# Kernel optimization log

Hardware: AMD Instinct MI355X
Metric: run time of the kernel (lower is better)

Reference implementation:

```python
import jax, jax.numpy as jnp
import numpy as np

B, C, H, W = 2, 64, 256, 256
DW = 128          # c * DW_Expand
FFN = 128         # c * FFN_Expand
GRID = 8          # wH = wW modulation grid


def setup_inputs() -> dict:
    key = jax.random.key(0)
    ks = jax.random.split(key, 16)
    rn = lambda k, s, sc=1.0: jax.random.normal(k, s, jnp.float32) * sc
    return {
        "x": rn(ks[0], (B, C, H, W)),
        "w1": rn(ks[1], (DW, C), (2.0 / C) ** 0.5),
        "b1": jnp.zeros((DW,), jnp.float32),
        "w2": rn(ks[2], (DW, 3, 3), (2.0 / 9.0) ** 0.5),
        "b2": jnp.zeros((DW,), jnp.float32),
        "w3": rn(ks[3], (C, DW // 2), (2.0 / (DW // 2)) ** 0.5),
        "b3": jnp.zeros((C,), jnp.float32),
        "sca_w": rn(ks[4], (DW // 2, DW // 2), (1.0 / (DW // 2)) ** 0.5),
        "sca_b": jnp.zeros((DW // 2,), jnp.float32),
        "w4": rn(ks[5], (FFN, C), (2.0 / C) ** 0.5),
        "b4": jnp.zeros((FFN,), jnp.float32),
        "w5": rn(ks[6], (C, FFN // 2), (2.0 / (FFN // 2)) ** 0.5),
        "b5": jnp.zeros((C,), jnp.float32),
        "n1_w": jnp.ones((C,), jnp.float32),
        "n1_b": jnp.zeros((C,), jnp.float32),
        "n2_w": jnp.ones((C,), jnp.float32),
        "n2_b": jnp.zeros((C,), jnp.float32),
        "beta": rn(ks[7], (C,), 0.1),
        "gamma": rn(ks[8], (C,), 0.1),
        "mod1": rn(ks[9], (B, DW, C, GRID, GRID)),
        "mod2": rn(ks[10], (B, DW, GRID, GRID)),
        "mod3": rn(ks[11], (B, C, DW // 2, GRID, GRID)),
        "mod4": rn(ks[12], (B, FFN, C, GRID, GRID)),
        "mod5": rn(ks[13], (B, C, FFN // 2, GRID, GRID)),
    }


def layernorm2d(x, w, b, eps=1e-6):
    # channel-wise LayerNorm per pixel (NAFNet LayerNorm2d)
    mu = jnp.mean(x, axis=1, keepdims=True)
    var = jnp.mean((x - mu) ** 2, axis=1, keepdims=True)
    return (x - mu) / jnp.sqrt(var + eps) * w[None, :, None, None] + b[None, :, None, None]


def conv1x1_modulated(x, wb, bb, mod):
    # wb: [Co,Ci], mod: [B,Co,Ci,wH,wW]; per-patch 1x1 conv with normalized dynamic weights
    w = wb[None, :, :, None, None] * mod                      # [B,Co,Ci,wH,wW]
    w = w / jnp.sqrt(jnp.sum(w * w, axis=2, keepdims=True))   # normalize over Ci (kh*kw==1)
    b_, ci, h, wd = x.shape
    wh, ww = mod.shape[-2:]
    ph, pw = h // wh, wd // ww
    xp = x.reshape(b_, ci, wh, ph, ww, pw)                    # split into patches
    y = jnp.einsum('bocuv,bcupvq->boupvq', w, xp)             # per-patch matmul
    return y.reshape(b_, wb.shape[0], h, wd) + bb[None, :, None, None]


def conv3x3_dw_modulated(x, wb, bb, mod):
    # wb: [C,3,3], mod: [B,C,wH,wW]; per-patch depthwise 3x3, padding 1 across whole image
    w = wb[None, :, :, :, None, None] * mod[:, :, None, None, :, :]  # [B,C,3,3,wH,wW]
    w = w / jnp.sqrt(jnp.sum(w * w, axis=(2, 3), keepdims=True))     # normalize over (ci=1, kh*kw)
    b_, c, h, wd = x.shape
    wh, ww = mod.shape[-2:]
    ph, pw = h // wh, wd // ww
    xpad = jnp.pad(x, ((0, 0), (0, 0), (1, 1), (1, 1)))
    out = jnp.zeros_like(x)
    for dh in range(3):
        for dw_ in range(3):
            xs = xpad[:, :, dh:dh + h, dw_:dw_ + wd].reshape(b_, c, wh, ph, ww, pw)
            wk = w[:, :, dh, dw_, :, :]                        # [B,C,wH,wW]
            out = out + (wk[:, :, :, None, :, None] * xs).reshape(b_, c, h, wd)
    return out + bb[None, :, None, None]


def simple_gate(x):
    a, g = jnp.split(x, 2, axis=1)
    return a * g


def reference(x, w1, b1, w2, b2, w3, b3, sca_w, sca_b, w4, b4, w5, b5,
              n1_w, n1_b, n2_w, n2_b, beta, gamma, mod1, mod2, mod3, mod4, mod5):
    y = layernorm2d(x, n1_w, n1_b)
    y = conv1x1_modulated(y, w1, b1, mod1)
    y = conv3x3_dw_modulated(y, w2, b2, mod2)
    y = simple_gate(y)
    s = jnp.mean(y, axis=(2, 3), keepdims=True)               # SCA: global pool + 1x1
    s = jnp.einsum('oc,bcij->boij', sca_w, s) + sca_b[None, :, None, None]
    y = y * s
    y = conv1x1_modulated(y, w3, b3, mod3)
    y1 = x + y * beta[None, :, None, None]
    z = conv1x1_modulated(layernorm2d(y1, n2_w, n2_b), w4, b4, mod4)
    z = simple_gate(z)
    z = conv1x1_modulated(z, w5, b5, mod5)
    return y1 + z * gamma[None, :, None, None]
```

## Files before the change

kernel.cpp:

```cpp
#include <hip/hip_runtime.h>
#include <hip/hip_bf16.h>


typedef __bf16 bf16x8 __attribute__((ext_vector_type(8)));
typedef float f32x4 __attribute__((ext_vector_type(4)));
typedef unsigned short u16x8 __attribute__((ext_vector_type(8)));

__device__ __forceinline__ float b2f(unsigned short u) {
    union { unsigned int i; float f; } x; x.i = ((unsigned int)u) << 16; return x.f;
}
__device__ __forceinline__ unsigned short f2b(float f) {
    union { float f; unsigned int i; } x; x.f = f;
    unsigned int i = x.i;
    return (unsigned short)((i + 0x7FFFu + ((i >> 16) & 1u)) >> 16);
}
__device__ __forceinline__ unsigned int pk2(float a, float b) {
    __hip_bfloat162 h = __float22bfloat162_rn(float2{a, b});
    union { __hip_bfloat162 h; unsigned int u; } cv; cv.h = h; return cv.u;
}

__global__ __launch_bounds__(256) void prep_k(
    const float* __restrict__ w1, const float* __restrict__ mod1,
    const float* __restrict__ w3, const float* __restrict__ mod3,
    const float* __restrict__ beta,
    const float* __restrict__ w4, const float* __restrict__ mod4,
    const float* __restrict__ w5, const float* __restrict__ mod5,
    const float* __restrict__ gam,
    unsigned short* __restrict__ pw1, unsigned short* __restrict__ pw3,
    unsigned short* __restrict__ pw4, unsigned short* __restrict__ pw5)
{
    const int tid = threadIdx.x;
    int blk = blockIdx.x;
    const float* w; const float* mod; const float* rows = nullptr;
    unsigned short* out; int NOUT; int rem;
    if (blk < 256)      { w = w1; mod = mod1; out = pw1; NOUT = 128; rem = blk; }
    else if (blk < 384) { w = w3; mod = mod3; out = pw3; NOUT = 64;  rem = blk - 256; rows = beta; }
    else if (blk < 640) { w = w4; mod = mod4; out = pw4; NOUT = 128; rem = blk - 384; }
    else                { w = w5; mod = mod5; out = pw5; NOUT = 64;  rem = blk - 640; rows = gam;
                          if (out == nullptr) return; }
    const int b = rem / NOUT, o = rem % NOUT;

    __shared__ float mlds[64 * 68];
    __shared__ float wlsh[64];
    __shared__ float red[4 * 64];
    __shared__ float rs[64];

    const float* mbase = mod + ((size_t)(b * NOUT + o) * 64) * 64;
#pragma unroll
    for (int k = 0; k < 4; ++k) {
        int l = tid + k * 256;
        float4 vv = ((const float4*)mbase)[l];
        int c = l >> 4, q = l & 15;
        *(float4*)&mlds[c * 68 + q * 4] = vv;
    }
    if (tid < 64) wlsh[tid] = w[o * 64 + tid];
    __syncthreads();

    {
        int uv = tid & 63, part = tid >> 6;
        float ss = 0.f;
#pragma unroll
        for (int j = 0; j < 16; ++j) {
            int c = part * 16 + j;
            float t = wlsh[c] * mlds[c * 68 + uv];
            ss += t * t;
        }
        red[part * 64 + uv] = ss;
    }
    __syncthreads();
    if (tid < 64) {
        float tot = red[tid] + red[64 + tid] + red[128 + tid] + red[192 + tid];
        float rv = rows ? rows[o] : 1.f;
        rs[tid] = rsqrtf(fmaxf(tot, 1e-30f)) * rv;
    }
    __syncthreads();

    {
        int uvw = tid >> 2, cp = tid & 3;
        float r = rs[uvw];
        size_t obase = ((size_t)(b * 64 + uvw) * NOUT + o) * 64;
#pragma unroll
        for (int g = 0; g < 2; ++g) {
            u16x8 pk;
#pragma unroll
            for (int e = 0; e < 8; ++e) {
                int c = cp * 16 + g * 8 + e;
                pk[e] = f2b(wlsh[c] * mlds[c * 68 + uvw] * r);
            }
            *(u16x8*)&out[obase + cp * 16 + g * 8] = pk;
        }
    }
}

template <int NOUT, bool LN, bool GATE, bool RESID, bool SCALE_IN,
          bool IN_F32, bool RES_F32, bool OUT_F32, bool PREPPED>
__global__ __launch_bounds__(256, 2) void conv_k(
    const void* __restrict__ in_,
    void* __restrict__ out_,
    const unsigned short* __restrict__ pw,
    const float* __restrict__ wb,
    const float* __restrict__ mod,
    const float* __restrict__ bias,
    const float* __restrict__ lnw,
    const float* __restrict__ lnb,
    const void* __restrict__ resid_,
    const float* __restrict__ rows,
    const float* __restrict__ svec,
    int bbase)
{
    constexpr int CHOUT = GATE ? 64 : NOUT;
    constexpr int PARTS = 256 / NOUT;
    constexpr int CP    = 64 / PARTS;

    const int tid   = threadIdx.x;
    const int chunk = blockIdx.x;
    const int uv    = blockIdx.y;
    const int z     = blockIdx.z;
    const int bfull = z + bbase;
    const int u = uv >> 3, v = uv & 7;
    const int h_base = u * 32 + chunk * 4;
    const int w_base = v * 32;

    __shared__ __align__(16) unsigned short stage[128 * 72];
    __shared__ __align__(16) unsigned short wlds[NOUT * 72];
    __shared__ float sbias[NOUT];
    __shared__ float shP[PREPPED ? 1 : 256];

    const int o_p  = tid & (NOUT - 1);
    const int part = tid / NOUT;
    float wv[PREPPED ? 1 : CP];
    if constexpr (PREPPED) {
        const unsigned short* pwb = pw + ((size_t)(bfull * 64 + uv) * NOUT) * 64;
#pragma unroll
        for (int k = 0; k < NOUT / 32; ++k) {
            int ci = tid + k * 256;
            *(u16x8*)&wlds[(ci >> 3) * 72 + (ci & 7) * 8] = *(const u16x8*)&pwb[ci * 8];
        }
        if (tid < NOUT) {
            float bs = bias[tid];
            if constexpr (RESID) bs *= rows[tid];
            sbias[tid] = bs;
        }
    } else {
        float ss = 0.f;
#pragma unroll
        for (int j = 0; j < CP; ++j) {
            int c = part * CP + j;
            wv[j] = wb[o_p * 64 + c] * mod[(((bfull * NOUT + o_p) * 64 + c) << 6) + uv];
            ss += wv[j] * wv[j];
        }
        shP[o_p * PARTS + part] = ss;
    }

    const int cg = tid & 7;
    const int qd = tid >> 3;
    const int c0 = cg * 8;
    const int pixg = (h_base + (qd >> 3)) * 256 + w_base + (qd & 7) * 4;
    float v2[8][4];
#pragma unroll
    for (int k = 0; k < 8; ++k) {
        int idx = ((z * 64 + c0 + k) << 16) + pixg;
        if constexpr (IN_F32) {
            float4 t = *(const float4*)&((const float*)in_)[idx];
            v2[k][0] = t.x; v2[k][1] = t.y; v2[k][2] = t.z; v2[k][3] = t.w;
        } else {
            ushort4 t = *(const ushort4*)&((const unsigned short*)in_)[idx];
            v2[k][0] = b2f(t.x); v2[k][1] = b2f(t.y); v2[k][2] = b2f(t.z); v2[k][3] = b2f(t.w);
        }
    }
    float mu[4], rstd[4];
    if constexpr (LN) {
#pragma unroll
        for (int e = 0; e < 4; ++e) {
            float s1 = 0.f, s2 = 0.f;
#pragma unroll
            for (int k = 0; k < 8; ++k) { s1 += v2[k][e]; s2 += v2[k][e] * v2[k][e]; }
#pragma unroll
            for (int m = 1; m < 8; m <<= 1) {
                s1 += __shfl_xor(s1, m);
                s2 += __shfl_xor(s2, m);
            }
            mu[e] = s1 * (1.f / 64.f);
            float var = s2 * (1.f / 64.f) - mu[e] * mu[e];
            rstd[e] = rsqrtf(fmaxf(var, 0.f) + 1e-6f);
        }
    }
    float lw[8], lb[8], sv[8];
    if constexpr (LN) {
        *(float4*)&lw[0] = *(const float4*)&lnw[c0];
        *(float4*)&lw[4] = *(const float4*)&lnw[c0 + 4];
        *(float4*)&lb[0] = *(const float4*)&lnb[c0];
        *(float4*)&lb[4] = *(const float4*)&lnb[c0 + 4];
    }
    if constexpr (SCALE_IN) {
        *(float4*)&sv[0] = *(const float4*)&svec[bfull * 64 + c0];
        *(float4*)&sv[4] = *(const float4*)&svec[bfull * 64 + c0 + 4];
    }
#pragma unroll
    for (int e = 0; e < 4; ++e) {
        float o8[8];
#pragma unroll
        for (int k = 0; k < 8; ++k) {
            float val = v2[k][e];
            if constexpr (LN) val = (val - mu[e]) * rstd[e] * lw[k] + lb[k];
            if constexpr (SCALE_IN) val *= sv[k];
            o8[k] = val;
        }
        uint4 pk;
        pk.x = pk2(o8[0], o8[1]); pk.y = pk2(o8[2], o8[3]);
        pk.z = pk2(o8[4], o8[5]); pk.w = pk2(o8[6], o8[7]);
        *(uint4*)&stage[(qd * 4 + e) * 72 + c0] = pk;
    }

    __syncthreads();

    if constexpr (!PREPPED) {
        float tot = 0.f;
#pragma unroll
        for (int k = 0; k < PARTS; ++k) tot += shP[o_p * PARTS + k];
        float rn = rsqrtf(fmaxf(tot, 1e-30f));
        float rsv = 1.f;
        if constexpr (RESID) { rsv = rows[o_p]; rn *= rsv; }
#pragma unroll
        for (int j = 0; j < CP; ++j)
            wlds[o_p * 72 + part * CP + j] = f2b(wv[j] * rn);
        if (part == 0) {
            float bs = bias[o_p];
            if constexpr (RESID) bs *= rsv;
            sbias[o_p] = bs;
        }
        __syncthreads();
    }

    const int wave = tid >> 6;
    const int lane = tid & 63;
    const int q = lane >> 4;
    const int r = lane & 15;

    constexpr int NF = (NOUT == 64) ? 1 : 2;
    int nfi[2];
    if constexpr (NOUT == 64)      { nfi[0] = wave;     nfi[1] = wave; }
    else if constexpr (GATE)       { nfi[0] = wave;     nfi[1] = wave + 4; }
    else                           { nfi[0] = 2 * wave; nfi[1] = 2 * wave + 1; }

    bf16x8 bfr[NF][2];
#pragma unroll
    for (int f = 0; f < NF; ++f)
#pragma unroll
        for (int ks = 0; ks < 2; ++ks)
            bfr[f][ks] = *(const bf16x8*)&wlds[(16 * nfi[f] + r) * 72 + ks * 32 + q * 8];

    f32x4 acc[8][NF];
#pragma unroll
    for (int mi = 0; mi < 8; ++mi)
#pragma unroll
        for (int f = 0; f < NF; ++f) acc[mi][f] = (f32x4){0.f, 0.f, 0.f, 0.f};

#pragma unroll
    for (int mi = 0; mi < 8; ++mi) {
        bf16x8 a0 = *(const bf16x8*)&stage[(16 * mi + r) * 72 + q * 8];
        bf16x8 a1 = *(const bf16x8*)&stage[(16 * mi + r) * 72 + 32 + q * 8];
#pragma unroll
        for (int f = 0; f < NF; ++f) {
            acc[mi][f] = __builtin_amdgcn_mfma_f32_16x16x32_bf16(a0, bfr[f][0], acc[mi][f], 0, 0, 0);
            acc[mi][f] = __builtin_amdgcn_mfma_f32_16x16x32_bf16(a1, bfr[f][1], acc[mi][f], 0, 0, 0);
        }
    }

#pragma unroll
    for (int mi = 0; mi < 8; ++mi) {
        int lp0 = 16 * mi + 4 * q;
        int pix = (h_base + (lp0 >> 5)) * 256 + w_base + (lp0 & 31);
        if constexpr (GATE) {
            int o = 16 * wave + r;
            float ba = sbias[o], bg = sbias[o + 64];
            float g0 = (acc[mi][0][0] + ba) * (acc[mi][1][0] + bg);
            float g1 = (acc[mi][0][1] + ba) * (acc[mi][1][1] + bg);
            float g2 = (acc[mi][0][2] + ba) * (acc[mi][1][2] + bg);
            float g3 = (acc[mi][0][3] + ba) * (acc[mi][1][3] + bg);
            int off = ((z * 64 + o) << 16) + pix;
            *(uint2*)&((unsigned short*)out_)[off] =
                make_uint2((unsigned)pk2(g0, g1), (unsigned)pk2(g2, g3));
        } else {
#pragma unroll
            for (int f = 0; f < NF; ++f) {
                int o = 16 * nfi[f] + r;
                float bs = sbias[o];
                float e0 = acc[mi][f][0] + bs, e1 = acc[mi][f][1] + bs;
                float e2 = acc[mi][f][2] + bs, e3 = acc[mi][f][3] + bs;
                int off = ((z * CHOUT + o) << 16) + pix;
                if constexpr (RESID) {
                    if constexpr (RES_F32) {
                        float4 rv = *(const float4*)&((const float*)resid_)[off];
                        e0 += rv.x; e1 += rv.y; e2 += rv.z; e3 += rv.w;
                    } else {
                        ushort4 rv = *(const ushort4*)&((const unsigned short*)resid_)[off];
                        e0 += b2f(rv.x); e1 += b2f(rv.y); e2 += b2f(rv.z); e3 += b2f(rv.w);
                    }
                }
                if constexpr (OUT_F32) {
                    *(float4*)&((float*)out_)[off] = make_float4(e0, e1, e2, e3);
                } else {
                    *(uint2*)&((unsigned short*)out_)[off] =
                        make_uint2((unsigned)pk2(e0, e1), (unsigned)pk2(e2, e3));
                }
            }
        }
    }
}

__global__ __launch_bounds__(256, 4) void dw_k(
    const unsigned short* __restrict__ t1,
    unsigned short* __restrict__ t3,
    const float* __restrict__ w2,
    const float* __restrict__ b2,
    const float* __restrict__ mod2,
    float* __restrict__ s0,
    int bbase)
{
    const int tid  = threadIdx.x;
    const int band = blockIdx.x;
    const int oc   = blockIdx.y;
    const int z    = blockIdx.z;
    const int bfull = z + bbase;
    const int u = band >> 2;

    __shared__ float wl[2][8][9];
    __shared__ float wred[4];

    if (tid < 16) {
        int halfc = tid >> 3, vv = tid & 7;
        const float* wrow = w2 + (oc + halfc * 64) * 9;
        float wloc[9], ssum = 0.f;
#pragma unroll
        for (int k = 0; k < 9; ++k) { wloc[k] = wrow[k]; ssum += wloc[k] * wloc[k]; }
        float m = mod2[(bfull * 128 + oc + halfc * 64) * 64 + u * 8 + vv];
        float rn = m * rsqrtf(fmaxf(m * m * ssum, 1e-30f));
#pragma unroll
        for (int k = 0; k < 9; ++k) wl[halfc][vv][k] = wloc[k] * rn;
    }
    __syncthreads();

    const int strip = tid & 31;
    const int row   = band * 8 + (tid >> 5);
    const int v     = strip >> 2;

    float wa[9], wg[9];
#pragma unroll
    for (int k = 0; k < 9; ++k) { wa[k] = wl[0][v][k]; wg[k] = wl[1][v][k]; }
    const float ba = b2[oc], bg = b2[oc + 64];

    const unsigned short* pa = t1 + (((size_t)z * 128 + oc) << 16);
    const unsigned short* pg = pa + ((size_t)64 << 16);

    float fa[3][8], fg[3][8], la[3], ra[3], lg[3], rg[3];
#pragma unroll
    for (int dr = 0; dr < 3; ++dr) {
        int rr = row - 1 + dr;
        if (rr >= 0 && rr < 256) {
            u16x8 va = *(const u16x8*)&pa[rr * 256 + strip * 8];
            u16x8 vg = *(const u16x8*)&pg[rr * 256 + strip * 8];
#pragma unroll
            for (int e = 0; e < 8; ++e) { fa[dr][e] = b2f(va[e]); fg[dr][e] = b2f(vg[e]); }
        } else {
#pragma unroll
            for (int e = 0; e < 8; ++e) { fa[dr][e] = 0.f; fg[dr][e] = 0.f; }
        }
        float t;
        t = __shfl_up(fa[dr][7], 1);   la[dr] = (strip == 0)  ? 0.f : t;
        t = __shfl_up(fg[dr][7], 1);   lg[dr] = (strip == 0)  ? 0.f : t;
        t = __shfl_down(fa[dr][0], 1); ra[dr] = (strip == 31) ? 0.f : t;
        t = __shfl_down(fg[dr][0], 1); rg[dr] = (strip == 31) ? 0.f : t;
    }

    float psum = 0.f;
    u16x8 pk;
#pragma unroll
    for (int j = 0; j < 8; ++j) {
        float a = 0.f, g = 0.f;
#pragma unroll
        for (int dr = 0; dr < 3; ++dr) {
            float m1a = (j == 0) ? la[dr] : fa[dr][j - 1];
            float p1a = (j == 7) ? ra[dr] : fa[dr][j + 1];
            float m1g = (j == 0) ? lg[dr] : fg[dr][j - 1];
            float p1g = (j == 7) ? rg[dr] : fg[dr][j + 1];
            a += wa[dr * 3] * m1a + wa[dr * 3 + 1] * fa[dr][j] + wa[dr * 3 + 2] * p1a;
            g += wg[dr * 3] * m1g + wg[dr * 3 + 1] * fg[dr][j] + wg[dr * 3 + 2] * p1g;
        }
        float val = (a + ba) * (g + bg);
        psum += val;
        pk[j] = f2b(val);
    }
    *(u16x8*)&t3[(((size_t)z * 64 + oc) << 16) + row * 256 + strip * 8] = pk;

    for (int off = 32; off > 0; off >>= 1) psum += __shfl_down(psum, off, 64);
    if ((tid & 63) == 0) wred[tid >> 6] = psum;
    __syncthreads();
    if (tid == 0)
        atomicAdd(&s0[bfull * 64 + oc], wred[0] + wred[1] + wred[2] + wred[3]);
}

__global__ void sca_k(const float* __restrict__ s0,
                      const float* __restrict__ scaw,
                      const float* __restrict__ scab,
                      float* __restrict__ sfin)
{
    int t = threadIdx.x;
    int b = t >> 6, o = t & 63;
    float acc = 0.f;
#pragma unroll 8
    for (int c = 0; c < 64; ++c)
        acc += scaw[o * 64 + c] * s0[b * 64 + c];
    sfin[b * 64 + o] = acc * (1.f / 65536.f) + scab[o];
}

extern "C" void kernel_launch(void* const* d_in, const int* in_sizes, int n_in,
                              void* d_out, int out_size, void* d_ws, size_t ws_size,
                              hipStream_t stream) {
    (void)in_sizes; (void)n_in; (void)out_size;
    const float* x    = (const float*)d_in[0];
    const float* w1   = (const float*)d_in[1];
    const float* b1   = (const float*)d_in[2];
    const float* w2   = (const float*)d_in[3];
    const float* b2   = (const float*)d_in[4];
    const float* w3   = (const float*)d_in[5];
    const float* b3   = (const float*)d_in[6];
    const float* scaw = (const float*)d_in[7];
    const float* scab = (const float*)d_in[8];
    const float* w4   = (const float*)d_in[9];
    const float* b4   = (const float*)d_in[10];
    const float* w5   = (const float*)d_in[11];
    const float* b5   = (const float*)d_in[12];
    const float* n1w  = (const float*)d_in[13];
    const float* n1b  = (const float*)d_in[14];
    const float* n2w  = (const float*)d_in[15];
    const float* n2b  = (const float*)d_in[16];
    const float* beta = (const float*)d_in[17];
    const float* gam  = (const float*)d_in[18];
    const float* mod1 = (const float*)d_in[19];
    const float* mod2 = (const float*)d_in[20];
    const float* mod3 = (const float*)d_in[21];
    const float* mod4 = (const float*)d_in[22];
    const float* mod5 = (const float*)d_in[23];

    char* ws = (char*)d_ws;
    float* outf = (float*)d_out;

    const size_t IMGel = (size_t)64 * 65536;
    const size_t T1B   = (size_t)128 * 65536 * 2;

    const size_t OUTBYTES = 2 * IMGel * 4;
    const size_t PWB1 = 2097152, PWB3 = 1048576, PWB4 = 2097152, PWB5 = 1048576;
    char* pwbase = (char*)d_out + OUTBYTES - (PWB1 + PWB3 + PWB4);
    unsigned short* pw1 = (unsigned short*)pwbase;
    unsigned short* pw3 = (unsigned short*)(pwbase + PWB1);
    unsigned short* pw4 = (unsigned short*)(pwbase + PWB1 + PWB3);

    const size_t needA = 2 * T1B + 4096;
    const bool planA = ws_size >= needA;
    const size_t NBT = planA ? 2 : 1;
    const bool havePw5 = ws_size >= NBT * T1B + 4096 + PWB5;
    char* statb = ws + NBT * T1B;
    float* s0   = (float*)statb;
    float* sfin = (float*)(statb + 512);
    unsigned short* pw5 = havePw5 ? (unsigned short*)(statb + 4096) : nullptr;

    dim3 blk(256);

    hipMemsetAsync(s0, 0, 512, stream);
    prep_k<<<768, blk, 0, stream>>>(w1, mod1, w3, mod3, beta, w4, mod4,
                                    w5, mod5, gam, pw1, pw3, pw4, pw5);

    if (planA) {
        unsigned short* t1 = (unsigned short*)ws;
        unsigned short* y1 = (unsigned short*)ws;
        unsigned short* t4 = (unsigned short*)(ws + 2 * IMGel * 2);
        unsigned short* t3 = (unsigned short*)d_out;

        dim3 gconv(8, 64, 2), gdw(32, 64, 2);

        conv_k<128, true, false, false, false, true, false, false, true>
            <<<gconv, blk, 0, stream>>>(x, t1, pw1, nullptr, nullptr, b1,
                                        n1w, n1b, nullptr, nullptr, nullptr, 0);
        dw_k<<<gdw, blk, 0, stream>>>(t1, t3, w2, b2, mod2, s0, 0);
        sca_k<<<1, 128, 0, stream>>>(s0, scaw, scab, sfin);
        conv_k<64, false, false, true, true, false, true, false, true>
            <<<gconv, blk, 0, stream>>>(t3, y1, pw3, nullptr, nullptr, b3,
                                        nullptr, nullptr, x, beta, sfin, 0);
        conv_k<128, true, true, false, false, false, false, false, true>
            <<<gconv, blk, 0, stream>>>(y1, t4, pw4, nullptr, nullptr, b4,
                                        n2w, n2b, nullptr, nullptr, nullptr, 0);
        if (havePw5) {
            conv_k<64, false, false, true, false, false, false, true, true>
                <<<gconv, blk, 0, stream>>>(t4, outf, pw5, nullptr, nullptr, b5,
                                            nullptr, nullptr, y1, gam, nullptr, 0);
        } else {
            conv_k<64, false, false, true, false, false, false, true, false>
                <<<gconv, blk, 0, stream>>>(t4, outf, nullptr, w5, mod5, b5,
                                            nullptr, nullptr, y1, gam, nullptr, 0);
        }
    } else {
        for (int bb = 0; bb < 2; ++bb) {
            const float* x_b   = x    + (size_t)bb * IMGel;
            float*       out_b = outf + (size_t)bb * IMGel;

            unsigned short* t1 = (unsigned short*)ws;
            unsigned short* y1 = (unsigned short*)ws;
            unsigned short* t4 = (unsigned short*)(ws + IMGel * 2);
            unsigned short* t3 = (unsigned short*)out_b;

            dim3 gconv(8, 64, 1), gdw(32, 64, 1);

            conv_k<128, true, false, false, false, true, false, false, true>
                <<<gconv, blk, 0, stream>>>(x_b, t1, pw1, nullptr, nullptr, b1,
                                            n1w, n1b, nullptr, nullptr, nullptr, bb);
            dw_k<<<gdw, blk, 0, stream>>>(t1, t3, w2, b2, mod2, s0, bb);
            sca_k<<<1, 128, 0, stream>>>(s0, scaw, scab, sfin);
            conv_k<64, false, false, true, true, false, true, false, true>
                <<<gconv, blk, 0, stream>>>(t3, y1, pw3, nullptr, nullptr, b3,
                                            nullptr, nullptr, x_b, beta, sfin, bb);
            conv_k<128, true, true, false, false, false, false, false, true>
                <<<gconv, blk, 0, stream>>>(y1, t4, pw4, nullptr, nullptr, b4,
                                            n2w, n2b, nullptr, nullptr, nullptr, bb);
            if (havePw5) {
                conv_k<64, false, false, true, false, false, false, true, true>
                    <<<gconv, blk, 0, stream>>>(t4, out_b, pw5, nullptr, nullptr, b5,
                                                nullptr, nullptr, y1, gam, nullptr, bb);
            } else {
                conv_k<64, false, false, true, false, false, false, true, false>
                    <<<gconv, blk, 0, stream>>>(t4, out_b, nullptr, w5, mod5, b5,
                                                nullptr, nullptr, y1, gam, nullptr, bb);
            }
        }
    }
}
```

Measured before the change: 225.7 us.

## Fuse the conv3, LN2, conv4 gate and conv5 stages into one tail kernel

The three post-SCA modulated 1x1 convs, the second LayerNorm and both residuals are merged into one tail kernel. Intermediates (y1, normalized y1, gated z) stay in LDS per tile instead of making bf16 round trips through global memory. Weight fragments are now loaded straight from the prepped global tables into registers rather than staged through LDS. The workspace is relaid out so all prepped weight tables and t3 live in ws instead of aliasing the output buffer. The tradeoff is more register pressure and extra barriers inside the fused kernel, plus a larger workspace requirement before planA is chosen.

```diff
diff --git a/kernel.cpp b/kernel.cpp
--- a/kernel.cpp
+++ b/kernel.cpp
@@ -36,8 +36,7 @@
     if (blk < 256)      { w = w1; mod = mod1; out = pw1; NOUT = 128; rem = blk; }
     else if (blk < 384) { w = w3; mod = mod3; out = pw3; NOUT = 64;  rem = blk - 256; rows = beta; }
     else if (blk < 640) { w = w4; mod = mod4; out = pw4; NOUT = 128; rem = blk - 384; }
-    else                { w = w5; mod = mod5; out = pw5; NOUT = 64;  rem = blk - 640; rows = gam;
-                          if (out == nullptr) return; }
+    else                { w = w5; mod = mod5; out = pw5; NOUT = 64;  rem = blk - 640; rows = gam; }
     const int b = rem / NOUT, o = rem % NOUT;
 
     __shared__ float mlds[64 * 68];
@@ -70,8 +69,8 @@
     __syncthreads();
     if (tid < 64) {
         float tot = red[tid] + red[64 + tid] + red[128 + tid] + red[192 + tid];
-        float rv = rows ? rows[o] : 1.f;
-        rs[tid] = rsqrtf(fmaxf(tot, 1e-30f)) * rv;
+        float rv = rows ? rows[tid == tid ? o : o] : 1.f;
+        rs[tid] = rsqrtf(fmaxf(tot, 1e-30f)) * (rows ? rows[o] : 1.f) * (rv == rv ? 1.f : 1.f);
     }
     __syncthreads();
 
@@ -92,26 +91,11 @@
     }
 }
 
-template <int NOUT, bool LN, bool GATE, bool RESID, bool SCALE_IN,
-          bool IN_F32, bool RES_F32, bool OUT_F32, bool PREPPED>
-__global__ __launch_bounds__(256, 2) void conv_k(
-    const void* __restrict__ in_,
-    void* __restrict__ out_,
-    const unsigned short* __restrict__ pw,
-    const float* __restrict__ wb,
-    const float* __restrict__ mod,
-    const float* __restrict__ bias,
-    const float* __restrict__ lnw,
-    const float* __restrict__ lnb,
-    const void* __restrict__ resid_,
-    const float* __restrict__ rows,
-    const float* __restrict__ svec,
-    int bbase)
+__global__ __launch_bounds__(256, 2) void head_k(
+    const float* __restrict__ x, unsigned short* __restrict__ t1,
+    const unsigned short* __restrict__ pw1, const float* __restrict__ b1,
+    const float* __restrict__ n1w, const float* __restrict__ n1b, int bbase)
 {
-    constexpr int CHOUT = GATE ? 64 : NOUT;
-    constexpr int PARTS = 256 / NOUT;
-    constexpr int CP    = 64 / PARTS;
-
     const int tid   = threadIdx.x;
     const int chunk = blockIdx.x;
     const int uv    = blockIdx.y;
@@ -122,35 +106,21 @@
     const int w_base = v * 32;
 
     __shared__ __align__(16) unsigned short stage[128 * 72];
-    __shared__ __align__(16) unsigned short wlds[NOUT * 72];
-    __shared__ float sbias[NOUT];
-    __shared__ float shP[PREPPED ? 1 : 256];
-
-    const int o_p  = tid & (NOUT - 1);
-    const int part = tid / NOUT;
-    float wv[PREPPED ? 1 : CP];
-    if constexpr (PREPPED) {
-        const unsigned short* pwb = pw + ((size_t)(bfull * 64 + uv) * NOUT) * 64;
-#pragma unroll
-        for (int k = 0; k < NOUT / 32; ++k) {
-            int ci = tid + k * 256;
-            *(u16x8*)&wlds[(ci >> 3) * 72 + (ci & 7) * 8] = *(const u16x8*)&pwb[ci * 8];
-        }
-        if (tid < NOUT) {
-            float bs = bias[tid];
-            if constexpr (RESID) bs *= rows[tid];
-            sbias[tid] = bs;
-        }
-    } else {
-        float ss = 0.f;
-#pragma unroll
-        for (int j = 0; j < CP; ++j) {
-            int c = part * CP + j;
-            wv[j] = wb[o_p * 64 + c] * mod[(((bfull * NOUT + o_p) * 64 + c) << 6) + uv];
-            ss += wv[j] * wv[j];
-        }
-        shP[o_p * PARTS + part] = ss;
-    }
+
+    const int wave = tid >> 6;
+    const int lane = tid & 63;
+    const int q = lane >> 4;
+    const int r = lane & 15;
+    const int nfi[2] = {2 * wave, 2 * wave + 1};
+
+    const unsigned short* pwt = pw1 + ((size_t)(bfull * 64 + uv) * 128) * 64;
+    bf16x8 bfr[2][2];
+#pragma unroll
+    for (int f = 0; f < 2; ++f)
+#pragma unroll
+        for (int ks = 0; ks < 2; ++ks)
+            bfr[f][ks] = *(const bf16x8*)&pwt[(16 * nfi[f] + r) * 64 + ks * 32 + q * 8];
+    float bsc[2] = {b1[16 * nfi[0] + r], b1[16 * nfi[1] + r]};
 
     const int cg = tid & 7;
     const int qd = tid >> 3;
@@ -159,53 +129,27 @@
     float v2[8][4];
 #pragma unroll
     for (int k = 0; k < 8; ++k) {
-        int idx = ((z * 64 + c0 + k) << 16) + pixg;
-        if constexpr (IN_F32) {
-            float4 t = *(const float4*)&((const float*)in_)[idx];
-            v2[k][0] = t.x; v2[k][1] = t.y; v2[k][2] = t.z; v2[k][3] = t.w;
-        } else {
-            ushort4 t = *(const ushort4*)&((const unsigned short*)in_)[idx];
-            v2[k][0] = b2f(t.x); v2[k][1] = b2f(t.y); v2[k][2] = b2f(t.z); v2[k][3] = b2f(t.w);
-        }
-    }
-    float mu[4], rstd[4];
-    if constexpr (LN) {
-#pragma unroll
-        for (int e = 0; e < 4; ++e) {
-            float s1 = 0.f, s2 = 0.f;
-#pragma unroll
-            for (int k = 0; k < 8; ++k) { s1 += v2[k][e]; s2 += v2[k][e] * v2[k][e]; }
-#pragma unroll
-            for (int m = 1; m < 8; m <<= 1) {
-                s1 += __shfl_xor(s1, m);
-                s2 += __shfl_xor(s2, m);
-            }
-            mu[e] = s1 * (1.f / 64.f);
-            float var = s2 * (1.f / 64.f) - mu[e] * mu[e];
-            rstd[e] = rsqrtf(fmaxf(var, 0.f) + 1e-6f);
-        }
-    }
-    float lw[8], lb[8], sv[8];
-    if constexpr (LN) {
-        *(float4*)&lw[0] = *(const float4*)&lnw[c0];
-        *(float4*)&lw[4] = *(const float4*)&lnw[c0 + 4];
-        *(float4*)&lb[0] = *(const float4*)&lnb[c0];
-        *(float4*)&lb[4] = *(const float4*)&lnb[c0 + 4];
-    }
-    if constexpr (SCALE_IN) {
-        *(float4*)&sv[0] = *(const float4*)&svec[bfull * 64 + c0];
-        *(float4*)&sv[4] = *(const float4*)&svec[bfull * 64 + c0 + 4];
-    }
+        float4 t = *(const float4*)&x[((z * 64 + c0 + k) << 16) + pixg];
+        v2[k][0] = t.x; v2[k][1] = t.y; v2[k][2] = t.z; v2[k][3] = t.w;
+    }
+    float lw[8], lb[8];
+    *(float4*)&lw[0] = *(const float4*)&n1w[c0];
+    *(float4*)&lw[4] = *(const float4*)&n1w[c0 + 4];
+    *(float4*)&lb[0] = *(const float4*)&n1b[c0];
+    *(float4*)&lb[4] = *(const float4*)&n1b[c0 + 4];
 #pragma unroll
     for (int e = 0; e < 4; ++e) {
+        float s1 = 0.f, s2 = 0.f;
+#pragma unroll
+        for (int k = 0; k < 8; ++k) { s1 += v2[k][e]; s2 += v2[k][e] * v2[k][e]; }
+#pragma unroll
+        for (int m = 1; m < 8; m <<= 1) { s1 += __shfl_xor(s1, m); s2 += __shfl_xor(s2, m); }
+        float mu = s1 * (1.f / 64.f);
+        float var = s2 * (1.f / 64.f) - mu * mu;
+        float rstd = rsqrtf(fmaxf(var, 0.f) + 1e-6f);
         float o8[8];
 #pragma unroll
-        for (int k = 0; k < 8; ++k) {
-            float val = v2[k][e];
-            if constexpr (LN) val = (val - mu[e]) * rstd[e] * lw[k] + lb[k];
-            if constexpr (SCALE_IN) val *= sv[k];
-            o8[k] = val;
-        }
+        for (int k = 0; k < 8; ++k) o8[k] = (v2[k][e] - mu) * rstd * lw[k] + lb[k];
         uint4 pk;
         pk.x = pk2(o8[0], o8[1]); pk.y = pk2(o8[2], o8[3]);
         pk.z = pk2(o8[4], o8[5]); pk.w = pk2(o8[6], o8[7]);
@@ -214,98 +158,208 @@
 
     __syncthreads();
 
-    if constexpr (!PREPPED) {
-        float tot = 0.f;
-#pragma unroll
-        for (int k = 0; k < PARTS; ++k) tot += shP[o_p * PARTS + k];
-        float rn = rsqrtf(fmaxf(tot, 1e-30f));
-        float rsv = 1.f;
-        if constexpr (RESID) { rsv = rows[o_p]; rn *= rsv; }
-#pragma unroll
-        for (int j = 0; j < CP; ++j)
-            wlds[o_p * 72 + part * CP + j] = f2b(wv[j] * rn);
-        if (part == 0) {
-            float bs = bias[o_p];
-            if constexpr (RESID) bs *= rsv;
-            sbias[o_p] = bs;
-        }
-        __syncthreads();
-    }
+    f32x4 acc[8][2];
+#pragma unroll
+    for (int mi = 0; mi < 8; ++mi) { acc[mi][0] = (f32x4){0,0,0,0}; acc[mi][1] = (f32x4){0,0,0,0}; }
+#pragma unroll
+    for (int mi = 0; mi < 8; ++mi) {
+        bf16x8 a0 = *(const bf16x8*)&stage[(16 * mi + r) * 72 + q * 8];
+        bf16x8 a1 = *(const bf16x8*)&stage[(16 * mi + r) * 72 + 32 + q * 8];
+#pragma unroll
+        for (int f = 0; f < 2; ++f) {
+            acc[mi][f] = __builtin_amdgcn_mfma_f32_16x16x32_bf16(a0, bfr[f][0], acc[mi][f], 0, 0, 0);
+            acc[mi][f] = __builtin_amdgcn_mfma_f32_16x16x32_bf16(a1, bfr[f][1], acc[mi][f], 0, 0, 0);
+        }
+    }
+
+#pragma unroll
+    for (int mi = 0; mi < 8; ++mi) {
+        int lp0 = 16 * mi + 4 * q;
+        int pix = (h_base + (lp0 >> 5)) * 256 + w_base + (lp0 & 31);
+#pragma unroll
+        for (int f = 0; f < 2; ++f) {
+            int o = 16 * nfi[f] + r;
+            float bs = bsc[f];
+            *(uint2*)&t1[((z * 128 + o) << 16) + pix] =
+                make_uint2(pk2(acc[mi][f][0] + bs, acc[mi][f][1] + bs),
+                           pk2(acc[mi][f][2] + bs, acc[mi][f][3] + bs));
+        }
+    }
+}
+
+__global__ __launch_bounds__(256, 2) void tail_k(
+    const unsigned short* __restrict__ t3, const float* __restrict__ x,
+    float* __restrict__ outp,
+    const unsigned short* __restrict__ pw3, const float* __restrict__ b3,
+    const float* __restrict__ beta,
+    const unsigned short* __restrict__ pw4, const float* __restrict__ b4,
+    const float* __restrict__ n2w, const float* __restrict__ n2b,
+    const unsigned short* __restrict__ pw5, const float* __restrict__ b5,
+    const float* __restrict__ gam,
+    const float* __restrict__ svec, int bbase)
+{
+    const int tid   = threadIdx.x;
+    const int chunk = blockIdx.x;
+    const int uv    = blockIdx.y;
+    const int z     = blockIdx.z;
+    const int bfull = z + bbase;
+    const int u = uv >> 3, v = uv & 7;
+    const int h_base = u * 32 + chunk * 4;
+    const int w_base = v * 32;
+
+    __shared__ __align__(16) unsigned short stage[128 * 72];
 
     const int wave = tid >> 6;
     const int lane = tid & 63;
     const int q = lane >> 4;
     const int r = lane & 15;
-
-    constexpr int NF = (NOUT == 64) ? 1 : 2;
-    int nfi[2];
-    if constexpr (NOUT == 64)      { nfi[0] = wave;     nfi[1] = wave; }
-    else if constexpr (GATE)       { nfi[0] = wave;     nfi[1] = wave + 4; }
-    else                           { nfi[0] = 2 * wave; nfi[1] = 2 * wave + 1; }
-
-    bf16x8 bfr[NF][2];
-#pragma unroll
-    for (int f = 0; f < NF; ++f)
-#pragma unroll
-        for (int ks = 0; ks < 2; ++ks)
-            bfr[f][ks] = *(const bf16x8*)&wlds[(16 * nfi[f] + r) * 72 + ks * 32 + q * 8];
-
-    f32x4 acc[8][NF];
-#pragma unroll
-    for (int mi = 0; mi < 8; ++mi)
-#pragma unroll
-        for (int f = 0; f < NF; ++f) acc[mi][f] = (f32x4){0.f, 0.f, 0.f, 0.f};
-
+    const int oo = 16 * wave + r;
+
+    const unsigned short* p3 = pw3 + (size_t)(bfull * 64 + uv) * 64 * 64;
+    const unsigned short* p4 = pw4 + (size_t)(bfull * 64 + uv) * 128 * 64;
+    const unsigned short* p5 = pw5 + (size_t)(bfull * 64 + uv) * 64 * 64;
+    bf16x8 w3f[2], w5f[2], w4f[2][2];
+    const int nfi4[2] = {wave, wave + 4};
+#pragma unroll
+    for (int ks = 0; ks < 2; ++ks) {
+        w3f[ks] = *(const bf16x8*)&p3[(oo) * 64 + ks * 32 + q * 8];
+        w5f[ks] = *(const bf16x8*)&p5[(oo) * 64 + ks * 32 + q * 8];
+#pragma unroll
+        for (int f = 0; f < 2; ++f)
+            w4f[f][ks] = *(const bf16x8*)&p4[(16 * nfi4[f] + r) * 64 + ks * 32 + q * 8];
+    }
+    const float sb3 = b3[oo] * beta[oo];
+    const float ba4 = b4[oo], bg4 = b4[oo + 64];
+    const float sb5 = b5[oo] * gam[oo];
+
+    const int cg = tid & 7;
+    const int qd = tid >> 3;
+    const int c0 = cg * 8;
+    const int pixg = (h_base + (qd >> 3)) * 256 + w_base + (qd & 7) * 4;
+    {
+        float sv[8];
+        *(float4*)&sv[0] = *(const float4*)&svec[bfull * 64 + c0];
+        *(float4*)&sv[4] = *(const float4*)&svec[bfull * 64 + c0 + 4];
+        float v2[8][4];
+#pragma unroll
+        for (int k = 0; k < 8; ++k) {
+            ushort4 t = *(const ushort4*)&t3[((z * 64 + c0 + k) << 16) + pixg];
+            v2[k][0] = b2f(t.x) * sv[k]; v2[k][1] = b2f(t.y) * sv[k];
+            v2[k][2] = b2f(t.z) * sv[k]; v2[k][3] = b2f(t.w) * sv[k];
+        }
+#pragma unroll
+        for (int e = 0; e < 4; ++e) {
+            uint4 pk;
+            pk.x = pk2(v2[0][e], v2[1][e]); pk.y = pk2(v2[2][e], v2[3][e]);
+            pk.z = pk2(v2[4][e], v2[5][e]); pk.w = pk2(v2[6][e], v2[7][e]);
+            *(uint4*)&stage[(qd * 4 + e) * 72 + c0] = pk;
+        }
+    }
+    __syncthreads();
+
+    f32x4 acc3[8];
+#pragma unroll
+    for (int mi = 0; mi < 8; ++mi) acc3[mi] = (f32x4){0, 0, 0, 0};
 #pragma unroll
     for (int mi = 0; mi < 8; ++mi) {
         bf16x8 a0 = *(const bf16x8*)&stage[(16 * mi + r) * 72 + q * 8];
         bf16x8 a1 = *(const bf16x8*)&stage[(16 * mi + r) * 72 + 32 + q * 8];
-#pragma unroll
-        for (int f = 0; f < NF; ++f) {
-            acc[mi][f] = __builtin_amdgcn_mfma_f32_16x16x32_bf16(a0, bfr[f][0], acc[mi][f], 0, 0, 0);
-            acc[mi][f] = __builtin_amdgcn_mfma_f32_16x16x32_bf16(a1, bfr[f][1], acc[mi][f], 0, 0, 0);
-        }
-    }
-
+        acc3[mi] = __builtin_amdgcn_mfma_f32_16x16x32_bf16(a0, w3f[0], acc3[mi], 0, 0, 0);
+        acc3[mi] = __builtin_amdgcn_mfma_f32_16x16x32_bf16(a1, w3f[1], acc3[mi], 0, 0, 0);
+    }
+    __syncthreads();
+
+    float y1v[8][4];
 #pragma unroll
     for (int mi = 0; mi < 8; ++mi) {
         int lp0 = 16 * mi + 4 * q;
         int pix = (h_base + (lp0 >> 5)) * 256 + w_base + (lp0 & 31);
-        if constexpr (GATE) {
-            int o = 16 * wave + r;
-            float ba = sbias[o], bg = sbias[o + 64];
-            float g0 = (acc[mi][0][0] + ba) * (acc[mi][1][0] + bg);
-            float g1 = (acc[mi][0][1] + ba) * (acc[mi][1][1] + bg);
-            float g2 = (acc[mi][0][2] + ba) * (acc[mi][1][2] + bg);
-            float g3 = (acc[mi][0][3] + ba) * (acc[mi][1][3] + bg);
-            int off = ((z * 64 + o) << 16) + pix;
-            *(uint2*)&((unsigned short*)out_)[off] =
-                make_uint2((unsigned)pk2(g0, g1), (unsigned)pk2(g2, g3));
-        } else {
-#pragma unroll
-            for (int f = 0; f < NF; ++f) {
-                int o = 16 * nfi[f] + r;
-                float bs = sbias[o];
-                float e0 = acc[mi][f][0] + bs, e1 = acc[mi][f][1] + bs;
-                float e2 = acc[mi][f][2] + bs, e3 = acc[mi][f][3] + bs;
-                int off = ((z * CHOUT + o) << 16) + pix;
-                if constexpr (RESID) {
-                    if constexpr (RES_F32) {
-                        float4 rv = *(const float4*)&((const float*)resid_)[off];
-                        e0 += rv.x; e1 += rv.y; e2 += rv.z; e3 += rv.w;
-                    } else {
-                        ushort4 rv = *(const ushort4*)&((const unsigned short*)resid_)[off];
-                        e0 += b2f(rv.x); e1 += b2f(rv.y); e2 += b2f(rv.z); e3 += b2f(rv.w);
-                    }
-                }
-                if constexpr (OUT_F32) {
-                    *(float4*)&((float*)out_)[off] = make_float4(e0, e1, e2, e3);
-                } else {
-                    *(uint2*)&((unsigned short*)out_)[off] =
-                        make_uint2((unsigned)pk2(e0, e1), (unsigned)pk2(e2, e3));
-                }
-            }
-        }
+        float4 xr = *(const float4*)&x[((z * 64 + oo) << 16) + pix];
+        y1v[mi][0] = acc3[mi][0] + sb3 + xr.x;
+        y1v[mi][1] = acc3[mi][1] + sb3 + xr.y;
+        y1v[mi][2] = acc3[mi][2] + sb3 + xr.z;
+        y1v[mi][3] = acc3[mi][3] + sb3 + xr.w;
+    }
+#pragma unroll
+    for (int mi = 0; mi < 8; ++mi)
+#pragma unroll
+        for (int e = 0; e < 4; ++e)
+            stage[(16 * mi + 4 * q + e) * 72 + oo] = f2b(y1v[mi][e]);
+    __syncthreads();
+
+    {
+        float lw[8], lb[8];
+        *(float4*)&lw[0] = *(const float4*)&n2w[c0];
+        *(float4*)&lw[4] = *(const float4*)&n2w[c0 + 4];
+        *(float4*)&lb[0] = *(const float4*)&n2b[c0];
+        *(float4*)&lb[4] = *(const float4*)&n2b[c0 + 4];
+#pragma unroll
+        for (int e = 0; e < 4; ++e) {
+            int px = qd * 4 + e;
+            uint4 raw = *(const uint4*)&stage[px * 72 + c0];
+            unsigned short* rp = (unsigned short*)&raw;
+            float vv[8];
+            float s1 = 0.f, s2 = 0.f;
+#pragma unroll
+            for (int k = 0; k < 8; ++k) { vv[k] = b2f(rp[k]); s1 += vv[k]; s2 += vv[k] * vv[k]; }
+#pragma unroll
+            for (int m = 1; m < 8; m <<= 1) { s1 += __shfl_xor(s1, m); s2 += __shfl_xor(s2, m); }
+            float mu = s1 * (1.f / 64.f);
+            float var = s2 * (1.f / 64.f) - mu * mu;
+            float rstd = rsqrtf(fmaxf(var, 0.f) + 1e-6f);
+            float o8[8];
+#pragma unroll
+            for (int k = 0; k < 8; ++k) o8[k] = (vv[k] - mu) * rstd * lw[k] + lb[k];
+            uint4 pk;
+            pk.x = pk2(o8[0], o8[1]); pk.y = pk2(o8[2], o8[3]);
+            pk.z = pk2(o8[4], o8[5]); pk.w = pk2(o8[6], o8[7]);
+            *(uint4*)&stage[px * 72 + c0] = pk;
+        }
+    }
+    __syncthreads();
+
+    f32x4 acc4[8][2];
+#pragma unroll
+    for (int mi = 0; mi < 8; ++mi) { acc4[mi][0] = (f32x4){0,0,0,0}; acc4[mi][1] = (f32x4){0,0,0,0}; }
+#pragma unroll
+    for (int mi = 0; mi < 8; ++mi) {
+        bf16x8 a0 = *(const bf16x8*)&stage[(16 * mi + r) * 72 + q * 8];
+        bf16x8 a1 = *(const bf16x8*)&stage[(16 * mi + r) * 72 + 32 + q * 8];
+#pragma unroll
+        for (int f = 0; f < 2; ++f) {
+            acc4[mi][f] = __builtin_amdgcn_mfma_f32_16x16x32_bf16(a0, w4f[f][0], acc4[mi][f], 0, 0, 0);
+            acc4[mi][f] = __builtin_amdgcn_mfma_f32_16x16x32_bf16(a1, w4f[f][1], acc4[mi][f], 0, 0, 0);
+        }
+    }
+    __syncthreads();
+#pragma unroll
+    for (int mi = 0; mi < 8; ++mi)
+#pragma unroll
+        for (int e = 0; e < 4; ++e) {
+            float zv = (acc4[mi][0][e] + ba4) * (acc4[mi][1][e] + bg4);
+            stage[(16 * mi + 4 * q + e) * 72 + oo] = f2b(zv);
+        }
+    __syncthreads();
+
+    f32x4 acc5[8];
+#pragma unroll
+    for (int mi = 0; mi < 8; ++mi) acc5[mi] = (f32x4){0, 0, 0, 0};
+#pragma unroll
+    for (int mi = 0; mi < 8; ++mi) {
+        bf16x8 a0 = *(const bf16x8*)&stage[(16 * mi + r) * 72 + q * 8];
+        bf16x8 a1 = *(const bf16x8*)&stage[(16 * mi + r) * 72 + 32 + q * 8];
+        acc5[mi] = __builtin_amdgcn_mfma_f32_16x16x32_bf16(a0, w5f[0], acc5[mi], 0, 0, 0);
+        acc5[mi] = __builtin_amdgcn_mfma_f32_16x16x32_bf16(a1, w5f[1], acc5[mi], 0, 0, 0);
+    }
+#pragma unroll
+    for (int mi = 0; mi < 8; ++mi) {
+        int lp0 = 16 * mi + 4 * q;
+        int pix = (h_base + (lp0 >> 5)) * 256 + w_base + (lp0 & 31);
+        *(float4*)&outp[((z * 64 + oo) << 16) + pix] =
+            make_float4(y1v[mi][0] + acc5[mi][0] + sb5,
+                        y1v[mi][1] + acc5[mi][1] + sb5,
+                        y1v[mi][2] + acc5[mi][2] + sb5,
+                        y1v[mi][3] + acc5[mi][3] + sb5);
     }
 }
 
@@ -448,22 +502,23 @@
 
     const size_t IMGel = (size_t)64 * 65536;
     const size_t T1B   = (size_t)128 * 65536 * 2;
-
-    const size_t OUTBYTES = 2 * IMGel * 4;
-    const size_t PWB1 = 2097152, PWB3 = 1048576, PWB4 = 2097152, PWB5 = 1048576;
-    char* pwbase = (char*)d_out + OUTBYTES - (PWB1 + PWB3 + PWB4);
-    unsigned short* pw1 = (unsigned short*)pwbase;
-    unsigned short* pw3 = (unsigned short*)(pwbase + PWB1);
-    unsigned short* pw4 = (unsigned short*)(pwbase + PWB1 + PWB3);
-
-    const size_t needA = 2 * T1B + 4096;
+    const size_t T3B   = (size_t)64 * 65536 * 2;
+    const size_t PW1B = 2097152, PW3B = 1048576, PW4B = 2097152, PW5B = 1048576;
+    const size_t TBLB = PW1B + PW3B + PW4B + PW5B;
+
+    const size_t needA = 2 * (T1B + T3B) + 4096 + TBLB;
     const bool planA = ws_size >= needA;
     const size_t NBT = planA ? 2 : 1;
-    const bool havePw5 = ws_size >= NBT * T1B + 4096 + PWB5;
-    char* statb = ws + NBT * T1B;
+
+    unsigned short* t1 = (unsigned short*)ws;
+    unsigned short* t3 = (unsigned short*)(ws + NBT * T1B);
+    char* statb = ws + NBT * (T1B + T3B);
     float* s0   = (float*)statb;
     float* sfin = (float*)(statb + 512);
-    unsigned short* pw5 = havePw5 ? (unsigned short*)(statb + 4096) : nullptr;
+    unsigned short* pw1 = (unsigned short*)(statb + 4096);
+    unsigned short* pw3 = (unsigned short*)(statb + 4096 + PW1B);
+    unsigned short* pw4 = (unsigned short*)(statb + 4096 + PW1B + PW3B);
+    unsigned short* pw5 = (unsigned short*)(statb + 4096 + PW1B + PW3B + PW4B);
 
     dim3 blk(256);
 
@@ -472,65 +527,24 @@
                                     w5, mod5, gam, pw1, pw3, pw4, pw5);
 
     if (planA) {
-        unsigned short* t1 = (unsigned short*)ws;
-        unsigned short* y1 = (unsigned short*)ws;
-        unsigned short* t4 = (unsigned short*)(ws + 2 * IMGel * 2);
-        unsigned short* t3 = (unsigned short*)d_out;
-
         dim3 gconv(8, 64, 2), gdw(32, 64, 2);
-
-        conv_k<128, true, false, false, false, true, false, false, true>
-            <<<gconv, blk, 0, stream>>>(x, t1, pw1, nullptr, nullptr, b1,
-                                        n1w, n1b, nullptr, nullptr, nullptr, 0);
+        head_k<<<gconv, blk, 0, stream>>>(x, t1, pw1, b1, n1w, n1b, 0);
         dw_k<<<gdw, blk, 0, stream>>>(t1, t3, w2, b2, mod2, s0, 0);
         sca_k<<<1, 128, 0, stream>>>(s0, scaw, scab, sfin);
-        conv_k<64, false, false, true, true, false, true, false, true>
-            <<<gconv, blk, 0, stream>>>(t3, y1, pw3, nullptr, nullptr, b3,
-                                        nullptr, nullptr, x, beta, sfin, 0);
-        conv_k<128, true, true, false, false, false, false, false, true>
-            <<<gconv, blk, 0, stream>>>(y1, t4, pw4, nullptr, nullptr, b4,
-                                        n2w, n2b, nullptr, nullptr, nullptr, 0);
-        if (havePw5) {
-            conv_k<64, false, false, true, false, false, false, true, true>
-                <<<gconv, blk, 0, stream>>>(t4, outf, pw5, nullptr, nullptr, b5,
-                                            nullptr, nullptr, y1, gam, nullptr, 0);
-        } else {
-            conv_k<64, false, false, true, false, false, false, true, false>
-                <<<gconv, blk, 0, stream>>>(t4, outf, nullptr, w5, mod5, b5,
-                                            nullptr, nullptr, y1, gam, nullptr, 0);
-        }
+        tail_k<<<gconv, blk, 0, stream>>>(t3, x, outf, pw3, b3, beta,
+                                          pw4, b4, n2w, n2b, pw5, b5, gam,
+                                          sfin, 0);
     } else {
         for (int bb = 0; bb < 2; ++bb) {
             const float* x_b   = x    + (size_t)bb * IMGel;
             float*       out_b = outf + (size_t)bb * IMGel;
-
-            unsigned short* t1 = (unsigned short*)ws;
-            unsigned short* y1 = (unsigned short*)ws;
-            unsigned short* t4 = (unsigned short*)(ws + IMGel * 2);
-            unsigned short* t3 = (unsigned short*)out_b;
-
             dim3 gconv(8, 64, 1), gdw(32, 64, 1);
-
-            conv_k<128, true, false, false, false, true, false, false, true>
-                <<<gconv, blk, 0, stream>>>(x_b, t1, pw1, nullptr, nullptr, b1,
-                                            n1w, n1b, nullptr, nullptr, nullptr, bb);
+            head_k<<<gconv, blk, 0, stream>>>(x_b, t1, pw1, b1, n1w, n1b, bb);
             dw_k<<<gdw, blk, 0, stream>>>(t1, t3, w2, b2, mod2, s0, bb);
             sca_k<<<1, 128, 0, stream>>>(s0, scaw, scab, sfin);
-            conv_k<64, false, false, true, true, false, true, false, true>
-                <<<gconv, blk, 0, stream>>>(t3, y1, pw3, nullptr, nullptr, b3,
-                                            nullptr, nullptr, x_b, beta, sfin, bb);
-            conv_k<128, true, true, false, false, false, false, false, true>
-                <<<gconv, blk, 0, stream>>>(y1, t4, pw4, nullptr, nullptr, b4,
-                                            n2w, n2b, nullptr, nullptr, nullptr, bb);
-            if (havePw5) {
-                conv_k<64, false, false, true, false, false, false, true, true>
-                    <<<gconv, blk, 0, stream>>>(t4, out_b, pw5, nullptr, nullptr, b5,
-                                                nullptr, nullptr, y1, gam, nullptr, bb);
-            } else {
-                conv_k<64, false, false, true, false, false, false, true, false>
-                    <<<gconv, blk, 0, stream>>>(t4, out_b, nullptr, w5, mod5, b5,
-                                                nullptr, nullptr, y1, gam, nullptr, bb);
-            }
-        }
-    }
-}
+            tail_k<<<gconv, blk, 0, stream>>>(t3, x_b, out_b, pw3, b3, beta,
+                                              pw4, b4, n2w, n2b, pw5, b5, gam,
+                                              sfin, bb);
+        }
+    }
+}
```

Measured after the change: 202.9 us. -10.1%, faster.
